# Kernel tuning notes

Hardware: AMD Instinct MI355X
Metric: run time of the kernel (lower is better)

## Reference

```python
import jax, jax.numpy as jnp
import numpy as np
from jax import lax

B, N, D, E, P, K, H = 32, 512, 512, 8, 96, 25, 4
PAD = 12  # conv padding so length is preserved


def setup_inputs() -> dict:
    key = jax.random.key(0)
    ks = jax.random.split(key, 16)
    s = 0.05  # weight scale to keep softmax/cosine well-conditioned
    x = jax.random.normal(ks[0], (B, N, D), dtype=jnp.float32)
    router = jax.random.normal(ks[1], (1, E, D), dtype=jnp.float32)
    Wq = jax.random.normal(ks[2], (D, D), dtype=jnp.float32) * s
    bq = jax.random.normal(ks[3], (D,), dtype=jnp.float32) * s
    Wk = jax.random.normal(ks[4], (D, D), dtype=jnp.float32) * s
    bk = jax.random.normal(ks[5], (D,), dtype=jnp.float32) * s
    Wv = jax.random.normal(ks[6], (D, D), dtype=jnp.float32) * s
    bv = jax.random.normal(ks[7], (D,), dtype=jnp.float32) * s
    Wo = jax.random.normal(ks[8], (D, D), dtype=jnp.float32) * s
    bo = jax.random.normal(ks[9], (D,), dtype=jnp.float32) * s
    Wc = jax.random.normal(ks[10], (E, 2, K), dtype=jnp.float32) * s  # E experts' Conv1d(2,1,25) stacked as out-channels
    bc = jax.random.normal(ks[11], (E,), dtype=jnp.float32) * s
    Wp = jax.random.normal(ks[12], (E, D, P), dtype=jnp.float32) * s  # E experts' Linear(D,P), stored (in,out)
    bp = jax.random.normal(ks[13], (E, P), dtype=jnp.float32) * s
    return {"x": x, "router": router, "Wq": Wq, "bq": bq, "Wk": Wk, "bk": bk,
            "Wv": Wv, "bv": bv, "Wo": Wo, "bo": bo, "Wc": Wc, "bc": bc,
            "Wp": Wp, "bp": bp}


def _forward(x, router, Wq, bq, Wk, bk, Wv, bv, Wo, bo, Wc, bc, Wp, bp):
    b, n, d = x.shape
    e = router.shape[1]
    dk = d // H
    r = jnp.broadcast_to(router, (b, e, d))
    # multi-head attention: queries=router slots, keys/values=x (dropout = identity at eval)
    q = (r @ Wq + bq).reshape(b, e, H, dk)
    k = (x @ Wk + bk).reshape(b, n, H, dk)
    v = (x @ Wv + bv).reshape(b, n, H, dk)
    scale = 1.0 / jnp.sqrt(jnp.asarray(dk, x.dtype))
    scores = jnp.einsum('blhe,bshe->bhls', q, k)  # [b,H,e,n]
    A = jax.nn.softmax(scale * scores, axis=-1)
    att = jnp.einsum('bhls,bshd->blhd', A, v).reshape(b, e, d)
    att = att @ Wo + bo  # [b,e,d]
    # cosine-similarity routing score, mapped to (1+pi)/2
    dot = jnp.einsum('bed,bnd->ben', att, x)
    norm_a = jnp.linalg.norm(att, axis=2, keepdims=True)          # [b,e,1]
    norm_x = jnp.linalg.norm(x, axis=2)[:, None, :]                # [b,1,n]
    score = (1.0 + dot / (norm_a * norm_x)) / 2.0                  # [b,e,n]
    idx = jnp.argmax(score, axis=1)                                # [b,n] expert per token
    z = jnp.take_along_axis(att, idx[:, :, None], axis=1)          # [b,n,d]
    result = jnp.stack([x, z], axis=-2).reshape(b * n, 2, d)       # [bn,2,d]
    # run all E expert convs at once (experts stacked as output channels)
    conv_out = lax.conv_general_dilated(
        result, Wc, window_strides=(1,), padding=[(PAD, PAD)],
        dimension_numbers=('NCH', 'OIH', 'NCH')) + bc[None, :, None]  # [bn,E,d]
    lin = jnp.einsum('nel,elp->nep', conv_out, Wp) + bp[None]         # [bn,E,P]
    flat_idx = idx.reshape(-1)
    out = jnp.take_along_axis(lin, flat_idx[:, None, None], axis=1)[:, 0, :]
    return out.reshape(b, n, P)


def reference(x, router, Wq, bq, Wk, bk, Wv, bv, Wo, bo, Wc, bc, Wp, bp):
    return _forward(x, router, Wq, bq, Wk, bk, Wv, bv, Wo, bo, Wc, bc, Wp, bp)
```

## Files before the change

### kernel.cpp

```cpp
#include <hip/hip_runtime.h>
#include <hip/hip_bf16.h>

#define B_ 32
#define N_ 512
#define D_ 512
#define E_ 8
#define P_ 96
#define KC 25
#define H_ 4
#define DK 128
#define HE 32
#define BN 16384

typedef short short8 __attribute__((ext_vector_type(8)));
typedef float f32x4 __attribute__((ext_vector_type(4)));

#define OCNT  4096
#define OS2   4352
#define OM    5120
#define OC    21504
#define OA    21536
#define OATT  676896
#define OTOK  807968
#define OWEFF 939040
#define OZC   1332256
#define OUP   1356832
#define OA1   5551136

__device__ __forceinline__ float b2f(short s) {
  unsigned u = ((unsigned)(unsigned short)s) << 16;
  return __builtin_bit_cast(float, u);
}
__device__ __forceinline__ unsigned short f2b(float f) {
  return __builtin_bit_cast(unsigned short, __float2bfloat16(f));
}

__global__ __launch_bounds__(256) void k_head(const float* __restrict__ router,
        const float* __restrict__ Wq, const float* __restrict__ bq,
        const float* __restrict__ Wk, const float* __restrict__ bk,
        const float* __restrict__ Wp, const float* __restrict__ Wc,
        float* __restrict__ M, float* __restrict__ c,
        int* __restrict__ cnt, float* __restrict__ s2,
        __hip_bfloat16* __restrict__ weff) {
  __shared__ float sm[5824];
  int bid = blockIdx.x;
  int tid = threadIdx.x;
  if (bid < 64) {
    float* rs = sm;
    float* ps = sm + 512;
    float* qs = sm + 768;
    int he = bid >> 1, ch = bid & 1;
    int h = he >> 3, e = he & 7;
    for (int i = tid; i < 512; i += 256) rs[i] = router[e * D_ + i];
    __syncthreads();
    {
      int j = tid & 127, dh = tid >> 7;
      const float* wq = Wq + h * 128 + j;
      float acc = 0.f;
      for (int d = dh * 256; d < dh * 256 + 256; d += 4) {
        acc = fmaf(rs[d], wq[d * D_], acc);
        acc = fmaf(rs[d + 1], wq[(d + 1) * D_], acc);
        acc = fmaf(rs[d + 2], wq[(d + 2) * D_], acc);
        acc = fmaf(rs[d + 3], wq[(d + 3) * D_], acc);
      }
      ps[dh * 128 + j] = acc;
    }
    __syncthreads();
    if (tid < 128) qs[tid] = ps[tid] + ps[128 + tid] + bq[h * 128 + tid];
    __syncthreads();
    {
      int d0 = ch * 256 + tid;
      const float* wrow = Wk + d0 * D_ + h * 128;
      float acc = 0.f;
      for (int jj = 0; jj < 128; jj += 4) {
        float4 wv = *(const float4*)(wrow + jj);
        acc = fmaf(wv.x, qs[jj], acc);
        acc = fmaf(wv.y, qs[jj + 1], acc);
        acc = fmaf(wv.z, qs[jj + 2], acc);
        acc = fmaf(wv.w, qs[jj + 3], acc);
      }
      M[he * D_ + d0] = acc;
    }
    if (ch == 0 && tid < 64) {
      float s = qs[tid] * bk[h * 128 + tid] + qs[tid + 64] * bk[h * 128 + tid + 64];
#pragma unroll
      for (int off = 32; off; off >>= 1) s += __shfl_xor(s, off);
      if (tid == 0) c[he] = s;
    }
  } else if (bid < 192) {
    float* T = sm;
    float* wcs = sm + 5760;
    int eb = bid - 64;
    int e = eb >> 4, mc = eb & 15;
    int lo = mc * 32 - 12;
    for (int idx = tid; idx < 56 * 24; idx += 256) {
      int lp = idx / 24, p4 = (idx - lp * 24) * 4;
      int l = lo + lp;
      float4 v = {0.f, 0.f, 0.f, 0.f};
      if (l >= 0 && l < D_) v = *(const float4*)(Wp + (e * D_ + l) * P_ + p4);
      T[p4 * 60 + lp] = v.x; T[(p4 + 1) * 60 + lp] = v.y;
      T[(p4 + 2) * 60 + lp] = v.z; T[(p4 + 3) * 60 + lp] = v.w;
    }
    if (tid < 50) wcs[tid] = Wc[e * 2 * KC + tid];
    __syncthreads();
    int m = tid & 31, pg = tid >> 5;
#pragma unroll
    for (int j = 0; j < 2; ++j)
      for (int k2 = 0; k2 < 12; ++k2) {
        int p = pg * 12 + k2;
        float acc = 0.f;
#pragma unroll
        for (int k = 0; k < KC; ++k)
          acc = fmaf(wcs[j * 25 + k], T[p * 60 + m - k + 24], acc);
        weff[(((e * 2 + j) * P_ + p) << 9) + mc * 32 + m] = __float2bfloat16(acc);
      }
  } else {
    int e = bid - 192;
    if (bid == 192) cnt[tid] = 0;
    if (tid < 192) {
      int p = tid % 96, lg = tid / 96;
      float s = 0.f;
      const float* wp = Wp + e * D_ * P_ + p;
      for (int l = lg * 256; l < lg * 256 + 256; ++l) s += wp[l * P_];
      sm[lg * 96 + p] = s;
    }
    __syncthreads();
    if (tid < 96) s2[e * 96 + tid] = sm[tid] + sm[96 + tid];
  }
}

__global__ __launch_bounds__(128) void k_logits(const float* __restrict__ x,
        const float* __restrict__ M, float* __restrict__ A0,
        float* __restrict__ A1) {
  __shared__ float xs[64 * 132];
  __shared__ float Ms[32 * 132];
  int dh = blockIdx.x & 1;
  int nt8 = (blockIdx.x >> 1) & 7;
  int b = blockIdx.x >> 4;
  int tid = threadIdx.x;
  const float* xb = x + (b * N_ + nt8 * 64) * D_ + dh * 256;
  const float* Mb = M + dh * 256;
  float acc[4][4] = {{0.f}};
  for (int kc = 0; kc < 2; ++kc) {
    for (int idx = tid; idx < 2048; idx += 128) {
      int r = idx >> 5, c4 = (idx & 31) * 4;
      *(float4*)(xs + r * 132 + c4) = *(const float4*)(xb + r * D_ + kc * 128 + c4);
    }
    for (int idx = tid; idx < 1024; idx += 128) {
      int r = idx >> 5, c4 = (idx & 31) * 4;
      *(float4*)(Ms + r * 132 + c4) = *(const float4*)(Mb + r * D_ + kc * 128 + c4);
    }
    __syncthreads();
    int nt = tid & 15, ht = tid >> 4;
#pragma unroll 4
    for (int d4 = 0; d4 < 128; d4 += 4) {
      float4 xv[4], mv[4];
#pragma unroll
      for (int i = 0; i < 4; ++i)
        xv[i] = *(const float4*)(xs + (nt + 16 * i) * 132 + d4);
#pragma unroll
      for (int j = 0; j < 4; ++j)
        mv[j] = *(const float4*)(Ms + (ht + 8 * j) * 132 + d4);
#pragma unroll
      for (int i = 0; i < 4; ++i)
#pragma unroll
        for (int j = 0; j < 4; ++j) {
          float s = acc[i][j];
          s = fmaf(xv[i].x, mv[j].x, s);
          s = fmaf(xv[i].y, mv[j].y, s);
          s = fmaf(xv[i].z, mv[j].z, s);
          s = fmaf(xv[i].w, mv[j].w, s);
          acc[i][j] = s;
        }
    }
    __syncthreads();
  }
  int nt = tid & 15, ht = tid >> 4;
  float* Ad = dh ? A1 : A0;
#pragma unroll
  for (int j = 0; j < 4; ++j) {
    int he = ht + 8 * j;
#pragma unroll
    for (int i = 0; i < 4; ++i)
      Ad[(b * HE + he) * N_ + nt8 * 64 + nt + 16 * i] = acc[i][j];
  }
}

__global__ __launch_bounds__(512) void k_u3(const float* __restrict__ x,
        const float* __restrict__ A0, const float* __restrict__ A1,
        const float* __restrict__ c, float* __restrict__ up) {
  __shared__ float As[64 * 33];
  __shared__ float mS[32], sS[32];
  int nq = blockIdx.x, b = blockIdx.y;
  int tid = threadIdx.x;
  const float scale = 0.08838834764831845f;
  {
    int wv = tid >> 6, lane = tid & 63;
    int he = wv * 4 + (lane >> 4);
    int l16 = lane & 15;
    const float* r0 = A0 + (b * HE + he) * N_;
    const float* r1 = A1 + (b * HE + he) * N_;
    float cc = c[he];
    float v[32];
    float m = -1e30f;
#pragma unroll
    for (int k = 0; k < 32; ++k) {
      int n = l16 + k * 16;
      float vv = scale * (r0[n] + r1[n] + cc);
      v[k] = vv;
      m = fmaxf(m, vv);
    }
    m = fmaxf(m, __shfl_xor(m, 1)); m = fmaxf(m, __shfl_xor(m, 2));
    m = fmaxf(m, __shfl_xor(m, 4)); m = fmaxf(m, __shfl_xor(m, 8));
    float s = 0.f;
#pragma unroll
    for (int k = 0; k < 32; ++k) s += expf(v[k] - m);
    s += __shfl_xor(s, 1); s += __shfl_xor(s, 2);
    s += __shfl_xor(s, 4); s += __shfl_xor(s, 8);
    if (l16 == 0) { mS[he] = m; sS[he] = 1.0f / s; }
  }
  __syncthreads();
  for (int idx = tid; idx < 64 * 32; idx += 512) {
    int n = idx & 63, he = idx >> 6;
    int gn = nq * 64 + n;
    float vv = scale * (A0[(b * HE + he) * N_ + gn] + A1[(b * HE + he) * N_ + gn]
                        + c[he]);
    As[n * 33 + he] = expf(vv - mS[he]) * sS[he];
  }
  __syncthreads();
  int dq = tid & 127, hg = tid >> 7;
  const float* xb = x + (b * N_ + nq * 64) * D_ + dq * 4;
  float acc[8][4];
#pragma unroll
  for (int j = 0; j < 8; ++j)
#pragma unroll
    for (int k = 0; k < 4; ++k) acc[j][k] = 0.f;
  for (int n = 0; n < 64; ++n) {
    float4 xv = *(const float4*)(xb + n * D_);
    const float* ar = As + n * 33 + hg * 8;
#pragma unroll
    for (int j = 0; j < 8; ++j) {
      float a = ar[j];
      acc[j][0] = fmaf(a, xv.x, acc[j][0]);
      acc[j][1] = fmaf(a, xv.y, acc[j][1]);
      acc[j][2] = fmaf(a, xv.z, acc[j][2]);
      acc[j][3] = fmaf(a, xv.w, acc[j][3]);
    }
  }
  float* o = up + (((b * 8 + nq) * HE) + hg * 8) * D_ + dq * 4;
#pragma unroll
  for (int j = 0; j < 8; ++j) {
    float4 v; v.x = acc[j][0]; v.y = acc[j][1]; v.z = acc[j][2]; v.w = acc[j][3];
    *(float4*)(o + j * D_) = v;
  }
}

__global__ __launch_bounds__(512) void k_vo3(const float* __restrict__ up,
        const float* __restrict__ Wv, const float* __restrict__ bv,
        const float* __restrict__ Wo, const float* __restrict__ bo,
        float* __restrict__ att) {
  __shared__ float us[4 * 512];
  __shared__ float part[4 * 512];
  __shared__ float ap_s[512];
  int b = blockIdx.x >> 3, e = blockIdx.x & 7;
  int tid = threadIdx.x;
  for (int idx = tid; idx < 4 * 128; idx += 512) {
    int h = idx >> 7, d4 = (idx & 127) * 4;
    const float* base = up + ((b * 8) * HE + h * 8 + e) * D_ + d4;
    float4 s = {0.f, 0.f, 0.f, 0.f};
#pragma unroll
    for (int nq = 0; nq < 8; ++nq) {
      float4 v = *(const float4*)(base + nq * HE * D_);
      s.x += v.x; s.y += v.y; s.z += v.z; s.w += v.w;
    }
    *(float4*)(us + h * 512 + d4) = s;
  }
  __syncthreads();
  {
    int cch = tid >> 7, j = tid & 127;
    int i0 = j * 4;
    int h = j >> 5;
    const float* ur = us + h * 512;
    const float* wv = Wv + i0;
    float4 acc = {0.f, 0.f, 0.f, 0.f};
    int d0 = cch * 128;
#pragma unroll 4
    for (int d = d0; d < d0 + 128; ++d) {
      float4 wq = *(const float4*)(wv + d * D_);
      float a = ur[d];
      acc.x = fmaf(a, wq.x, acc.x);
      acc.y = fmaf(a, wq.y, acc.y);
      acc.z = fmaf(a, wq.z, acc.z);
      acc.w = fmaf(a, wq.w, acc.w);
    }
    *(float4*)(part + cch * 512 + i0) = acc;
  }
  __syncthreads();
  ap_s[tid] = part[tid] + part[512 + tid] + part[1024 + tid] + part[1536 + tid]
              + bv[tid];
  __syncthreads();
  {
    int cch = tid >> 7, j = tid & 127;
    int o0 = j * 4;
    const float* wo = Wo + o0;
    float4 acc = {0.f, 0.f, 0.f, 0.f};
    int i0 = cch * 128;
#pragma unroll 4
    for (int i = i0; i < i0 + 128; ++i) {
      float4 wq = *(const float4*)(wo + i * D_);
      float a = ap_s[i];
      acc.x = fmaf(a, wq.x, acc.x);
      acc.y = fmaf(a, wq.y, acc.y);
      acc.z = fmaf(a, wq.z, acc.z);
      acc.w = fmaf(a, wq.w, acc.w);
    }
    *(float4*)(part + cch * 512 + o0) = acc;
  }
  __syncthreads();
  att[(b * E_ + e) * D_ + tid] = part[tid] + part[512 + tid] + part[1024 + tid]
                                 + part[1536 + tid] + bo[tid];
}

__global__ __launch_bounds__(256) void k_route2(const float* __restrict__ x,
        const float* __restrict__ att, const __hip_bfloat16* __restrict__ weff,
        const float* __restrict__ s2, const float* __restrict__ bc,
        const float* __restrict__ bp, int* __restrict__ cnt,
        int* __restrict__ tok, float* __restrict__ zc) {
  __shared__ float att_s[8 * D_];
  __shared__ float rn[8];
  __shared__ float red[4][520];
  __shared__ int blist[8][32];
  __shared__ int bcnt[8];
  int b = blockIdx.x >> 4, tile = blockIdx.x & 15;
  for (int idx = threadIdx.x; idx < 1024; idx += 256)
    *(float4*)(att_s + idx * 4) = *(const float4*)(att + b * E_ * D_ + idx * 4);
  if (threadIdx.x < 8) bcnt[threadIdx.x] = 0;
  __syncthreads();
  {
    int e = threadIdx.x >> 5, l = threadIdx.x & 31;
    float s = 0.f;
    for (int d0 = l; d0 < D_; d0 += 32) {
      float v = att_s[e * D_ + d0];
      s = fmaf(v, v, s);
    }
#pragma unroll
    for (int off = 16; off; off >>= 1) s += __shfl_xor(s, off);
    if (l == 0) rn[e] = 1.0f / sqrtf(s);
  }
  __syncthreads();
  int w = threadIdx.x >> 6, lane = threadIdx.x & 63;
  int e2 = lane & 7, ch = lane >> 3;
  float* rw = red[w];
  for (int i = 0; i < 8; ++i) {
    int t = b * N_ + tile * 32 + w * 8 + i;
    const float* xp = x + t * D_ + lane * 8;
    float4 xa = *(const float4*)xp;
    float4 xb4 = *(const float4*)(xp + 4);
    float p[8];
#pragma unroll
    for (int e = 0; e < 8; ++e) {
      const float* apt = att_s + e * D_ + lane * 8;
      float4 a0 = *(const float4*)apt;
      float4 a1 = *(const float4*)(apt + 4);
      float s = a0.x * xa.x;
      s = fmaf(a0.y, xa.y, s); s = fmaf(a0.z, xa.z, s); s = fmaf(a0.w, xa.w, s);
      s = fmaf(a1.x, xb4.x, s); s = fmaf(a1.y, xb4.y, s);
      s = fmaf(a1.z, xb4.z, s); s = fmaf(a1.w, xb4.w, s);
      p[e] = s;
    }
#pragma unroll
    for (int e = 0; e < 8; ++e) rw[e * 65 + lane] = p[e];
    float s = 0.f;
#pragma unroll
    for (int k = 0; k < 8; ++k) s += rw[e2 * 65 + ch * 8 + k];
    s += __shfl_xor(s, 8); s += __shfl_xor(s, 16); s += __shfl_xor(s, 32);
    float sc = s * rn[e2];
    int be = e2;
#pragma unroll
    for (int off = 1; off < 8; off <<= 1) {
      float o = __shfl_xor(sc, off);
      int oe = __shfl_xor(be, off);
      if (o > sc || (o == sc && oe < be)) { sc = o; be = oe; }
    }
    if (lane == 0) {
      int slot = atomicAdd(&bcnt[be], 1);
      blist[be][slot] = t;
    }
  }
  __syncthreads();
  {
    int e = threadIdx.x >> 5, r = threadIdx.x & 31;
    int ce = bcnt[e];
    int gs = 0;
    if (r == 0 && ce > 0) gs = atomicAdd(&cnt[e * 32], ce);
    gs = __shfl(gs, (threadIdx.x & 63) & 32);
    for (int k2 = r; k2 < ce; k2 += 32) tok[e * BN + gs + k2] = blist[e][k2];
  }
  int grp = threadIdx.x >> 4, l16 = threadIdx.x & 15;
  for (int r = 0; r < 3; ++r) {
    int P = tile * 48 + r * 16 + grp;
    int ez = P / 96, p = P - ez * 96;
    const short* wrow = (const short*)weff + (((ez * 2 + 1) * P_ + p) << 9);
    const float* arow = att_s + ez * D_;
    float acc = 0.f;
#pragma unroll
    for (int seg = 0; seg < 4; ++seg) {
      int d = seg * 128 + l16 * 8;
      short8 w8 = *(const short8*)(wrow + d);
      const float* a8 = arow + d;
      acc = fmaf(a8[0], b2f(w8[0]), acc); acc = fmaf(a8[1], b2f(w8[1]), acc);
      acc = fmaf(a8[2], b2f(w8[2]), acc); acc = fmaf(a8[3], b2f(w8[3]), acc);
      acc = fmaf(a8[4], b2f(w8[4]), acc); acc = fmaf(a8[5], b2f(w8[5]), acc);
      acc = fmaf(a8[6], b2f(w8[6]), acc); acc = fmaf(a8[7], b2f(w8[7]), acc);
    }
    acc += __shfl_xor(acc, 1); acc += __shfl_xor(acc, 2);
    acc += __shfl_xor(acc, 4); acc += __shfl_xor(acc, 8);
    if (l16 == 0)
      zc[(b * E_ + ez) * P_ + p] = acc + bc[ez] * s2[ez * 96 + p] + bp[ez * 96 + p];
  }
}

__global__ __launch_bounds__(256) void k_final(const float* __restrict__ x,
        const __hip_bfloat16* __restrict__ weff, const float* __restrict__ zc,
        const int* __restrict__ cnt, const int* __restrict__ tok,
        float* __restrict__ out) {
  __shared__ __align__(16) unsigned short xsb[32 * 520];
  __shared__ int toks[32];
  int g = blockIdx.x;
  int cl_e[E_], bs[E_ + 1];
  bs[0] = 0;
#pragma unroll
  for (int e = 0; e < E_; ++e) {
    cl_e[e] = cnt[e * 32];
    bs[e + 1] = bs[e] + ((cl_e[e] + 31) >> 5);
  }
  if (g >= bs[E_]) return;
  int e = 0;
#pragma unroll
  for (int k = 1; k < E_; ++k) if (g >= bs[k]) e = k;
  int base = (g - bs[e]) * 32;
  int cnt_e = cl_e[e];
  int cl = cnt_e - base; if (cl > 32) cl = 32;
  int tid = threadIdx.x;
  if (tid < 32) toks[tid] = (tid < cl) ? tok[e * BN + base + tid] : tok[e * BN + base];
  __syncthreads();
  for (int idx = tid; idx < 32 * 128; idx += 256) {
    int r = idx >> 7, c4 = (idx & 127) * 4;
    float4 v = *(const float4*)(x + toks[r] * D_ + c4);
    ushort4 u4;
    u4.x = f2b(v.x); u4.y = f2b(v.y); u4.z = f2b(v.z); u4.w = f2b(v.w);
    *(ushort4*)(xsb + r * 520 + c4) = u4;
  }
  __syncthreads();
  int wave = tid >> 6, lane = tid & 63;
  int mw = wave & 1, nw = wave >> 1;
  int m16 = lane & 15, quad = lane >> 4;
  const short* w0 = (const short*)(weff + (e * 2 + 0) * P_ * D_);
  f32x4 acc[3];
#pragma unroll
  for (int nt = 0; nt < 3; ++nt) acc[nt] = (f32x4){0.f, 0.f, 0.f, 0.f};
  const short* arow = (const short*)xsb + (mw * 16 + m16) * 520 + quad * 8;
  const short* brow = w0 + (nw * 48 + m16) * D_ + quad * 8;
  for (int kt = 0; kt < 16; ++kt) {
    int koff = kt * 32;
    short8 a = *(const short8*)(arow + koff);
#pragma unroll
    for (int nt = 0; nt < 3; ++nt) {
      short8 bf = *(const short8*)(brow + nt * 16 * D_ + koff);
      acc[nt] = __builtin_amdgcn_mfma_f32_16x16x32_bf16(a, bf, acc[nt], 0, 0, 0);
    }
  }
#pragma unroll
  for (int nt = 0; nt < 3; ++nt)
#pragma unroll
    for (int rr = 0; rr < 4; ++rr) {
      int row = mw * 16 + quad * 4 + rr;
      if (row < cl) {
        int tg = toks[row];
        int bb = tg >> 9;
        int p = nw * 48 + nt * 16 + m16;
        out[tg * P_ + p] = acc[nt][rr] + zc[(bb * E_ + e) * P_ + p];
      }
    }
}

extern "C" void kernel_launch(void* const* d_in, const int* in_sizes, int n_in,
                              void* d_out, int out_size, void* d_ws, size_t ws_size,
                              hipStream_t stream) {
  const float* x      = (const float*)d_in[0];
  const float* router = (const float*)d_in[1];
  const float* Wq     = (const float*)d_in[2];
  const float* bq     = (const float*)d_in[3];
  const float* Wk     = (const float*)d_in[4];
  const float* bk     = (const float*)d_in[5];
  const float* Wv     = (const float*)d_in[6];
  const float* bv     = (const float*)d_in[7];
  const float* Wo     = (const float*)d_in[8];
  const float* bo     = (const float*)d_in[9];
  const float* Wc     = (const float*)d_in[10];
  const float* bc     = (const float*)d_in[11];
  const float* Wp     = (const float*)d_in[12];
  const float* bp     = (const float*)d_in[13];
  float* out = (float*)d_out;
  float* w = (float*)d_ws;

  int*   cnt  = (int*)(w + OCNT);
  float* s2   = w + OS2;
  float* M    = w + OM;
  float* c    = w + OC;
  float* A0   = w + OA;
  float* A1   = w + OA1;
  float* att  = w + OATT;
  int*   tok  = (int*)(w + OTOK);
  __hip_bfloat16* weff = (__hip_bfloat16*)(w + OWEFF);
  float* zc   = w + OZC;
  float* up   = w + OUP;

  k_head<<<200, 256, 0, stream>>>(router, Wq, bq, Wk, bk, Wp, Wc, M, c, cnt, s2, weff);
  k_logits<<<512, 128, 0, stream>>>(x, M, A0, A1);
  k_u3<<<dim3(8, 32), 512, 0, stream>>>(x, A0, A1, c, up);
  k_vo3<<<256, 512, 0, stream>>>(up, Wv, bv, Wo, bo, att);
  k_route2<<<512, 256, 0, stream>>>(x, att, weff, s2, bc, bp, cnt, tok, zc);
  k_final<<<520, 256, 0, stream>>>(x, weff, zc, cnt, tok, out);
}
```

Baseline: 223.2 us.

## Fuse Wv projection into attention-weighted sum and split Wo into separate kernel

Restructures the attention value path. Each k_u block now handles one batch, one head and four experts over all tokens, computing softmax, A·x and the Wv head slice in one kernel. This removes the large per-chunk partial 'up' buffer and its reduction pass. The Wo projection moves to a new k_op kernel that processes four experts per block, so each Wo column slice is reused across four experts. The trade-off is that each k_u block now streams the whole x[b] from memory, and per-block shared memory grows to about 48KB.

```diff
diff --git a/kernel.cpp b/kernel.cpp
--- a/kernel.cpp
+++ b/kernel.cpp
@@ -24,8 +24,8 @@
 #define OTOK  807968
 #define OWEFF 939040
 #define OZC   1332256
-#define OUP   1356832
 #define OA1   5551136
+#define OAP   16777216
 
 __device__ __forceinline__ float b2f(short s) {
   unsigned u = ((unsigned)(unsigned short)s) << 16;
@@ -186,139 +186,186 @@
   }
 }
 
-__global__ __launch_bounds__(512) void k_u3(const float* __restrict__ x,
+__global__ __launch_bounds__(512) void k_u(const float* __restrict__ x,
         const float* __restrict__ A0, const float* __restrict__ A1,
-        const float* __restrict__ c, float* __restrict__ up) {
-  __shared__ float As[64 * 33];
-  __shared__ float mS[32], sS[32];
-  int nq = blockIdx.x, b = blockIdx.y;
+        const float* __restrict__ c, const float* __restrict__ Wv,
+        const float* __restrict__ bv, float* __restrict__ ap) {
+  __shared__ __align__(16) char smem[49248];
+  float* Ast  = (float*)smem;
+  float* part = (float*)(smem + 8192);
+  float* ust  = (float*)(smem + 40960);
+  float* mH   = (float*)(smem + 49152);
+  float* sH   = (float*)(smem + 49184);
+  float* mS   = (float*)(smem + 49216);
+  float* iS   = (float*)(smem + 49232);
+  int id = blockIdx.x;
+  int b = id & 31, g = id >> 5;
+  int h = g >> 1, eb = (g & 1) * 4;
   int tid = threadIdx.x;
   const float scale = 0.08838834764831845f;
-  {
-    int wv = tid >> 6, lane = tid & 63;
-    int he = wv * 4 + (lane >> 4);
-    int l16 = lane & 15;
-    const float* r0 = A0 + (b * HE + he) * N_;
-    const float* r1 = A1 + (b * HE + he) * N_;
-    float cc = c[he];
-    float v[32];
+  int wv = tid >> 6, lane = tid & 63;
+  int he_l = wv >> 1, half = wv & 1;
+  {
+    int heg = g * 4 + he_l;
+    const float* r0 = A0 + (b * HE + heg) * N_;
+    const float* r1 = A1 + (b * HE + heg) * N_;
+    float cc = c[heg];
+    float v[4];
     float m = -1e30f;
 #pragma unroll
-    for (int k = 0; k < 32; ++k) {
-      int n = l16 + k * 16;
+    for (int k = 0; k < 4; ++k) {
+      int n = half * 256 + lane + k * 64;
       float vv = scale * (r0[n] + r1[n] + cc);
       v[k] = vv;
       m = fmaxf(m, vv);
     }
     m = fmaxf(m, __shfl_xor(m, 1)); m = fmaxf(m, __shfl_xor(m, 2));
     m = fmaxf(m, __shfl_xor(m, 4)); m = fmaxf(m, __shfl_xor(m, 8));
+    m = fmaxf(m, __shfl_xor(m, 16)); m = fmaxf(m, __shfl_xor(m, 32));
+    if (lane == 0) mH[wv] = m;
+    __syncthreads();
+    m = fmaxf(mH[he_l * 2], mH[he_l * 2 + 1]);
+    if (lane == 0 && half == 0) mS[he_l] = m;
     float s = 0.f;
 #pragma unroll
-    for (int k = 0; k < 32; ++k) s += expf(v[k] - m);
-    s += __shfl_xor(s, 1); s += __shfl_xor(s, 2);
-    s += __shfl_xor(s, 4); s += __shfl_xor(s, 8);
-    if (l16 == 0) { mS[he] = m; sS[he] = 1.0f / s; }
-  }
-  __syncthreads();
-  for (int idx = tid; idx < 64 * 32; idx += 512) {
-    int n = idx & 63, he = idx >> 6;
-    int gn = nq * 64 + n;
-    float vv = scale * (A0[(b * HE + he) * N_ + gn] + A1[(b * HE + he) * N_ + gn]
-                        + c[he]);
-    As[n * 33 + he] = expf(vv - mS[he]) * sS[he];
-  }
-  __syncthreads();
-  int dq = tid & 127, hg = tid >> 7;
-  const float* xb = x + (b * N_ + nq * 64) * D_ + dq * 4;
-  float acc[8][4];
-#pragma unroll
-  for (int j = 0; j < 8; ++j)
-#pragma unroll
-    for (int k = 0; k < 4; ++k) acc[j][k] = 0.f;
-  for (int n = 0; n < 64; ++n) {
-    float4 xv = *(const float4*)(xb + n * D_);
-    const float* ar = As + n * 33 + hg * 8;
-#pragma unroll
-    for (int j = 0; j < 8; ++j) {
-      float a = ar[j];
-      acc[j][0] = fmaf(a, xv.x, acc[j][0]);
-      acc[j][1] = fmaf(a, xv.y, acc[j][1]);
-      acc[j][2] = fmaf(a, xv.z, acc[j][2]);
-      acc[j][3] = fmaf(a, xv.w, acc[j][3]);
-    }
-  }
-  float* o = up + (((b * 8 + nq) * HE) + hg * 8) * D_ + dq * 4;
-#pragma unroll
-  for (int j = 0; j < 8; ++j) {
-    float4 v; v.x = acc[j][0]; v.y = acc[j][1]; v.z = acc[j][2]; v.w = acc[j][3];
-    *(float4*)(o + j * D_) = v;
-  }
-}
-
-__global__ __launch_bounds__(512) void k_vo3(const float* __restrict__ up,
-        const float* __restrict__ Wv, const float* __restrict__ bv,
+    for (int k = 0; k < 4; ++k) s += expf(v[k] - m);
+    s += __shfl_xor(s, 1); s += __shfl_xor(s, 2); s += __shfl_xor(s, 4);
+    s += __shfl_xor(s, 8); s += __shfl_xor(s, 16); s += __shfl_xor(s, 32);
+    if (lane == 0) sH[wv] = s;
+    __syncthreads();
+    if (lane == 0 && half == 0) iS[he_l] = 1.0f / (sH[he_l * 2] + sH[he_l * 2 + 1]);
+  }
+  __syncthreads();
+  for (int idx = tid; idx < 2048; idx += 512) {
+    int hl = idx >> 9, n = idx & 511;
+    int heg = g * 4 + hl;
+    float vv = scale * (A0[(b * HE + heg) * N_ + n] + A1[(b * HE + heg) * N_ + n]
+                        + c[heg]);
+    Ast[n * 4 + hl] = expf(vv - mS[hl]) * iS[hl];
+  }
+  __syncthreads();
+  {
+    int ns = tid >> 7, dg = tid & 127;
+    float4 acc[4];
+#pragma unroll
+    for (int j = 0; j < 4; ++j) acc[j] = (float4){0.f, 0.f, 0.f, 0.f};
+    const float* xb = x + (b * N_ + ns * 128) * D_ + dg * 4;
+    const float* ab = Ast + ns * 128 * 4;
+#pragma unroll 4
+    for (int n = 0; n < 128; ++n) {
+      float4 xv = *(const float4*)(xb + n * D_);
+      float4 av = *(const float4*)(ab + n * 4);
+      acc[0].x = fmaf(av.x, xv.x, acc[0].x); acc[0].y = fmaf(av.x, xv.y, acc[0].y);
+      acc[0].z = fmaf(av.x, xv.z, acc[0].z); acc[0].w = fmaf(av.x, xv.w, acc[0].w);
+      acc[1].x = fmaf(av.y, xv.x, acc[1].x); acc[1].y = fmaf(av.y, xv.y, acc[1].y);
+      acc[1].z = fmaf(av.y, xv.z, acc[1].z); acc[1].w = fmaf(av.y, xv.w, acc[1].w);
+      acc[2].x = fmaf(av.z, xv.x, acc[2].x); acc[2].y = fmaf(av.z, xv.y, acc[2].y);
+      acc[2].z = fmaf(av.z, xv.z, acc[2].z); acc[2].w = fmaf(av.z, xv.w, acc[2].w);
+      acc[3].x = fmaf(av.w, xv.x, acc[3].x); acc[3].y = fmaf(av.w, xv.y, acc[3].y);
+      acc[3].z = fmaf(av.w, xv.z, acc[3].z); acc[3].w = fmaf(av.w, xv.w, acc[3].w);
+    }
+#pragma unroll
+    for (int j = 0; j < 4; ++j)
+      *(float4*)(part + ns * 2048 + j * 512 + dg * 4) = acc[j];
+  }
+  __syncthreads();
+  {
+    int d = tid;
+    float4 s = {0.f, 0.f, 0.f, 0.f};
+#pragma unroll
+    for (int ns2 = 0; ns2 < 4; ++ns2) {
+      s.x += part[ns2 * 2048 + 0 * 512 + d];
+      s.y += part[ns2 * 2048 + 1 * 512 + d];
+      s.z += part[ns2 * 2048 + 2 * 512 + d];
+      s.w += part[ns2 * 2048 + 3 * 512 + d];
+    }
+    *(float4*)(ust + d * 4) = s;
+  }
+  __syncthreads();
+  {
+    int kq = tid >> 5, cg = tid & 31, c4 = cg * 4;
+    float4 a2[4];
+#pragma unroll
+    for (int j = 0; j < 4; ++j) a2[j] = (float4){0.f, 0.f, 0.f, 0.f};
+    const float* wvp = Wv + h * 128 + c4;
+#pragma unroll 4
+    for (int d = kq * 32; d < kq * 32 + 32; ++d) {
+      float4 w4 = *(const float4*)(wvp + d * D_);
+      float4 uu = *(const float4*)(ust + d * 4);
+      a2[0].x = fmaf(uu.x, w4.x, a2[0].x); a2[0].y = fmaf(uu.x, w4.y, a2[0].y);
+      a2[0].z = fmaf(uu.x, w4.z, a2[0].z); a2[0].w = fmaf(uu.x, w4.w, a2[0].w);
+      a2[1].x = fmaf(uu.y, w4.x, a2[1].x); a2[1].y = fmaf(uu.y, w4.y, a2[1].y);
+      a2[1].z = fmaf(uu.y, w4.z, a2[1].z); a2[1].w = fmaf(uu.y, w4.w, a2[1].w);
+      a2[2].x = fmaf(uu.z, w4.x, a2[2].x); a2[2].y = fmaf(uu.z, w4.y, a2[2].y);
+      a2[2].z = fmaf(uu.z, w4.z, a2[2].z); a2[2].w = fmaf(uu.z, w4.w, a2[2].w);
+      a2[3].x = fmaf(uu.w, w4.x, a2[3].x); a2[3].y = fmaf(uu.w, w4.y, a2[3].y);
+      a2[3].z = fmaf(uu.w, w4.z, a2[3].z); a2[3].w = fmaf(uu.w, w4.w, a2[3].w);
+    }
+#pragma unroll
+    for (int j = 0; j < 4; ++j)
+      *(float4*)(part + kq * 512 + j * 128 + c4) = a2[j];
+  }
+  __syncthreads();
+  {
+    int j = tid >> 7, cc = tid & 127;
+    float s = 0.f;
+#pragma unroll
+    for (int kq2 = 0; kq2 < 16; ++kq2) s += part[kq2 * 512 + j * 128 + cc];
+    ap[(b * E_ + eb + j) * D_ + h * 128 + cc] = s + bv[h * 128 + cc];
+  }
+}
+
+__global__ __launch_bounds__(512) void k_op(const float* __restrict__ ap,
         const float* __restrict__ Wo, const float* __restrict__ bo,
         float* __restrict__ att) {
-  __shared__ float us[4 * 512];
-  __shared__ float part[4 * 512];
-  __shared__ float ap_s[512];
-  int b = blockIdx.x >> 3, e = blockIdx.x & 7;
+  __shared__ __align__(16) char smem[40960];
+  float* apt  = (float*)smem;
+  float* part = (float*)(smem + 8192);
+  int id = blockIdx.x;
+  int b = id & 31, q2 = id >> 5;
+  int cq = q2 >> 1, eh = q2 & 1;
   int tid = threadIdx.x;
-  for (int idx = tid; idx < 4 * 128; idx += 512) {
-    int h = idx >> 7, d4 = (idx & 127) * 4;
-    const float* base = up + ((b * 8) * HE + h * 8 + e) * D_ + d4;
-    float4 s = {0.f, 0.f, 0.f, 0.f};
-#pragma unroll
-    for (int nq = 0; nq < 8; ++nq) {
-      float4 v = *(const float4*)(base + nq * HE * D_);
-      s.x += v.x; s.y += v.y; s.z += v.z; s.w += v.w;
-    }
-    *(float4*)(us + h * 512 + d4) = s;
-  }
-  __syncthreads();
-  {
-    int cch = tid >> 7, j = tid & 127;
-    int i0 = j * 4;
-    int h = j >> 5;
-    const float* ur = us + h * 512;
-    const float* wv = Wv + i0;
-    float4 acc = {0.f, 0.f, 0.f, 0.f};
-    int d0 = cch * 128;
+  {
+    int j = tid >> 7, tl = tid & 127;
+    const float* arow = ap + (b * E_ + eh * 4 + j) * D_;
+#pragma unroll
+    for (int k = 0; k < 4; ++k) {
+      int i = tl + k * 128;
+      apt[i * 4 + j] = arow[i];
+    }
+  }
+  __syncthreads();
+  {
+    int kq = tid >> 5, cg = tid & 31, c4 = cg * 4;
+    float4 a2[4];
+#pragma unroll
+    for (int j = 0; j < 4; ++j) a2[j] = (float4){0.f, 0.f, 0.f, 0.f};
+    const float* wop = Wo + cq * 128 + c4;
 #pragma unroll 4
-    for (int d = d0; d < d0 + 128; ++d) {
-      float4 wq = *(const float4*)(wv + d * D_);
-      float a = ur[d];
-      acc.x = fmaf(a, wq.x, acc.x);
-      acc.y = fmaf(a, wq.y, acc.y);
-      acc.z = fmaf(a, wq.z, acc.z);
-      acc.w = fmaf(a, wq.w, acc.w);
-    }
-    *(float4*)(part + cch * 512 + i0) = acc;
-  }
-  __syncthreads();
-  ap_s[tid] = part[tid] + part[512 + tid] + part[1024 + tid] + part[1536 + tid]
-              + bv[tid];
-  __syncthreads();
-  {
-    int cch = tid >> 7, j = tid & 127;
-    int o0 = j * 4;
-    const float* wo = Wo + o0;
-    float4 acc = {0.f, 0.f, 0.f, 0.f};
-    int i0 = cch * 128;
-#pragma unroll 4
-    for (int i = i0; i < i0 + 128; ++i) {
-      float4 wq = *(const float4*)(wo + i * D_);
-      float a = ap_s[i];
-      acc.x = fmaf(a, wq.x, acc.x);
-      acc.y = fmaf(a, wq.y, acc.y);
-      acc.z = fmaf(a, wq.z, acc.z);
-      acc.w = fmaf(a, wq.w, acc.w);
-    }
-    *(float4*)(part + cch * 512 + o0) = acc;
-  }
-  __syncthreads();
-  att[(b * E_ + e) * D_ + tid] = part[tid] + part[512 + tid] + part[1024 + tid]
-                                 + part[1536 + tid] + bo[tid];
+    for (int d = kq * 32; d < kq * 32 + 32; ++d) {
+      float4 w4 = *(const float4*)(wop + d * D_);
+      float4 uu = *(const float4*)(apt + d * 4);
+      a2[0].x = fmaf(uu.x, w4.x, a2[0].x); a2[0].y = fmaf(uu.x, w4.y, a2[0].y);
+      a2[0].z = fmaf(uu.x, w4.z, a2[0].z); a2[0].w = fmaf(uu.x, w4.w, a2[0].w);
+      a2[1].x = fmaf(uu.y, w4.x, a2[1].x); a2[1].y = fmaf(uu.y, w4.y, a2[1].y);
+      a2[1].z = fmaf(uu.y, w4.z, a2[1].z); a2[1].w = fmaf(uu.y, w4.w, a2[1].w);
+      a2[2].x = fmaf(uu.z, w4.x, a2[2].x); a2[2].y = fmaf(uu.z, w4.y, a2[2].y);
+      a2[2].z = fmaf(uu.z, w4.z, a2[2].z); a2[2].w = fmaf(uu.z, w4.w, a2[2].w);
+      a2[3].x = fmaf(uu.w, w4.x, a2[3].x); a2[3].y = fmaf(uu.w, w4.y, a2[3].y);
+      a2[3].z = fmaf(uu.w, w4.z, a2[3].z); a2[3].w = fmaf(uu.w, w4.w, a2[3].w);
+    }
+#pragma unroll
+    for (int j = 0; j < 4; ++j)
+      *(float4*)(part + kq * 512 + j * 128 + c4) = a2[j];
+  }
+  __syncthreads();
+  {
+    int j = tid >> 7, cc = tid & 127;
+    float s = 0.f;
+#pragma unroll
+    for (int kq2 = 0; kq2 < 16; ++kq2) s += part[kq2 * 512 + j * 128 + cc];
+    att[(b * E_ + eh * 4 + j) * D_ + cq * 128 + cc] = s + bo[cq * 128 + cc];
+  }
 }
 
 __global__ __launch_bounds__(256) void k_route2(const float* __restrict__ x,
@@ -514,12 +561,12 @@
   int*   tok  = (int*)(w + OTOK);
   __hip_bfloat16* weff = (__hip_bfloat16*)(w + OWEFF);
   float* zc   = w + OZC;
-  float* up   = w + OUP;
+  float* ap   = w + OAP;
 
   k_head<<<200, 256, 0, stream>>>(router, Wq, bq, Wk, bk, Wp, Wc, M, c, cnt, s2, weff);
   k_logits<<<512, 128, 0, stream>>>(x, M, A0, A1);
-  k_u3<<<dim3(8, 32), 512, 0, stream>>>(x, A0, A1, c, up);
-  k_vo3<<<256, 512, 0, stream>>>(up, Wv, bv, Wo, bo, att);
+  k_u<<<256, 512, 0, stream>>>(x, A0, A1, c, Wv, bv, ap);
+  k_op<<<256, 512, 0, stream>>>(ap, Wo, bo, att);
   k_route2<<<512, 256, 0, stream>>>(x, att, weff, s2, bc, bp, cnt, tok, zc);
   k_final<<<520, 256, 0, stream>>>(x, weff, zc, cnt, tok, out);
 }
```

Result: faster. 208.7 us (-6.5%).
